# Kernel optimization log

Measured on AMD Instinct MI355X. Metric: run time of the kernel, lower is better.

## Reference

```python
import jax, jax.numpy as jnp
import numpy as np

DIM = 2048
N_HEADS = 32
N_KV_HEADS = 8
HEAD_DIM = 64
ROPE_BASE = 10000.0
BATCH = 2
SEQ = 2048


def apply_rope(x, cos, sin):
    # x: (B, S, H, hd); cos/sin: (1, S, 1, hd//2). Interleaved rotation.
    x1 = x[..., ::2]
    x2 = x[..., 1::2]
    r1 = x1 * cos - x2 * sin
    r2 = x1 * sin + x2 * cos
    return jnp.stack([r1, r2], axis=-1).reshape(x.shape)


def setup_inputs() -> dict:
    key = jax.random.key(0)
    ks = jax.random.split(key, 8)
    s = DIM ** -0.5
    x = jax.random.normal(ks[0], (BATCH, SEQ, DIM), dtype=jnp.float32)
    Wq = jax.random.normal(ks[1], (DIM, N_HEADS * HEAD_DIM), dtype=jnp.float32) * s
    Wk = jax.random.normal(ks[2], (DIM, N_KV_HEADS * HEAD_DIM), dtype=jnp.float32) * s
    Wv = jax.random.normal(ks[3], (DIM, N_KV_HEADS * HEAD_DIM), dtype=jnp.float32) * s
    bv = jax.random.normal(ks[4], (N_KV_HEADS * HEAD_DIM,), dtype=jnp.float32) * 0.01
    Wo = jax.random.normal(ks[5], (N_HEADS * HEAD_DIM, DIM), dtype=jnp.float32) * s
    bo = jax.random.normal(ks[6], (DIM,), dtype=jnp.float32) * 0.01
    # causal mask: 1 where attended, 0 where masked
    mask = jnp.tril(jnp.ones((SEQ, SEQ), dtype=jnp.int32))[None, None]
    return {"x": x, "Wq": Wq, "Wk": Wk, "Wv": Wv, "bv": bv, "Wo": Wo, "bo": bo, "mask": mask}


def reference(x, Wq, Wk, Wv, bv, Wo, bo, mask):
    B, S, _ = x.shape
    q = (x @ Wq).reshape(B, S, N_HEADS, HEAD_DIM)
    k = (x @ Wk).reshape(B, S, N_KV_HEADS, HEAD_DIM)
    v = (x @ Wv + bv).reshape(B, S, N_KV_HEADS, HEAD_DIM)

    # RoPE tables
    theta = 1.0 / ROPE_BASE ** (jnp.arange(0, HEAD_DIM, 2, dtype=jnp.float32) / HEAD_DIM)
    freqs = jnp.arange(S, dtype=jnp.float32)[:, None] * theta[None, :]  # (S, hd/2)
    cos = jnp.cos(freqs)[None, :, None, :]
    sin = jnp.sin(freqs)[None, :, None, :]

    q = apply_rope(q, cos, sin)
    k = apply_rope(k, cos, sin)

    rf = N_HEADS // N_KV_HEADS
    k = jnp.repeat(k, rf, axis=2)  # materialized GQA repeat, as in source
    v = jnp.repeat(v, rf, axis=2)

    scale = HEAD_DIM ** -0.5
    scores = jnp.einsum("bqhd,bkhd->bhqk", q, k) * scale  # (B, H, S, S)
    scores = jnp.where(mask == 0, -jnp.inf, scores)
    attn = jax.nn.softmax(scores, axis=-1)
    out = jnp.einsum("bhqk,bkhd->bqhd", attn, v).reshape(B, S, N_HEADS * HEAD_DIM)
    return out @ Wo + bo
```

## Files before the change

kernel.cpp:

```cpp
#include <hip/hip_runtime.h>
#include <hip/hip_bf16.h>

#define DIMX     2048
#define N_HEADS  32
#define N_KVH    8
#define HEAD_D   64
#define BATCH    2
#define SEQ      2048
#define M_ROWS   (BATCH * SEQ)
#define QKVN     3072
#define THETA_C  0.2878231366242557f
#define C1SCALE  0.1803368801111204f

typedef __attribute__((ext_vector_type(8))) short short8;
typedef __attribute__((ext_vector_type(4))) float f32x4;

#define DEV static __device__ __forceinline__

DEV float b2f(unsigned short u) { return __uint_as_float(((unsigned int)u) << 16); }
DEV unsigned short f2b(float f) {
  unsigned int x = __float_as_uint(f);
  return (unsigned short)((x + 0x7fffu + ((x >> 16) & 1u)) >> 16);
}
DEV unsigned int pk2(float lo, float hi) {
  __hip_bfloat162 h = __float22bfloat162_rn(make_float2(lo, hi));
  unsigned int u;
  __builtin_memcpy(&u, &h, 4);
  return u;
}
DEV void gld16(const void* g, void* lds) {
  __builtin_amdgcn_global_load_lds(
      (const __attribute__((address_space(1))) unsigned int*)g,
      (__attribute__((address_space(3))) unsigned int*)lds, 16, 0, 0);
}

__global__ void tab_k(float2* __restrict__ tab)
{
  int i = blockIdx.x * 256 + threadIdx.x;
  int s = i >> 5, j = i & 31;
  float th = __expf(-(float)j * THETA_C);
  float sn, cs;
  sincosf((float)s * th, &sn, &cs);
  tab[i] = make_float2(cs, sn);
}

__global__ void cast_k(const float* __restrict__ s, unsigned short* __restrict__ d, int n8)
{
  int i = blockIdx.x * 256 + threadIdx.x;
  if (i >= n8) return;
  float4 a = ((const float4*)s)[i * 2];
  float4 b = ((const float4*)s)[i * 2 + 1];
  uint4 o;
  o.x = pk2(a.x, a.y); o.y = pk2(a.z, a.w);
  o.z = pk2(b.x, b.y); o.w = pk2(b.z, b.w);
  ((uint4*)d)[i] = o;
}

__global__ __launch_bounds__(256) void transcast_k(
    const float* __restrict__ W, unsigned short* __restrict__ Wt, int Kd, int N)
{
  __shared__ float tile[64][65];
  const int t = threadIdx.x;
  const int k0 = blockIdx.y * 64, n0 = blockIdx.x * 64;
  const int r = t >> 4, c4 = (t & 15) << 2;
  #pragma unroll
  for (int pp = 0; pp < 4; ++pp) {
    float4 v = *(const float4*)(W + (size_t)(k0 + pp * 16 + r) * N + n0 + c4);
    *(float4*)&tile[pp * 16 + r][c4] = v;
  }
  __syncthreads();
  const int n = t >> 2, kc = (t & 3) << 4;
  uint4 u0, u1;
  u0.x = pk2(tile[kc + 0][n], tile[kc + 1][n]);
  u0.y = pk2(tile[kc + 2][n], tile[kc + 3][n]);
  u0.z = pk2(tile[kc + 4][n], tile[kc + 5][n]);
  u0.w = pk2(tile[kc + 6][n], tile[kc + 7][n]);
  u1.x = pk2(tile[kc + 8][n], tile[kc + 9][n]);
  u1.y = pk2(tile[kc + 10][n], tile[kc + 11][n]);
  u1.z = pk2(tile[kc + 12][n], tile[kc + 13][n]);
  u1.w = pk2(tile[kc + 14][n], tile[kc + 15][n]);
  unsigned short* dst = Wt + (size_t)(n0 + n) * Kd + k0 + kc;
  *(uint4*)dst = u0;
  *(uint4*)(dst + 8) = u1;
}

#define TM 128
#define TK 32

template<int OUTB>
__global__ __launch_bounds__(256) void gemm_bf16_k(
    const unsigned short* __restrict__ A,
    const unsigned short* __restrict__ Bt,
    const float* __restrict__ bias,
    void* __restrict__ Cp, int M, int N, int K)
{
  __shared__ unsigned short Al[TM * TK];
  __shared__ unsigned short Bl[TM * TK];
  const int t = threadIdx.x;
  const int l = t & 63, w = t >> 6;
  const int col = l & 15, grp = l >> 4;
  const int wr = (w >> 1) * 64, wc = (w & 1) * 64;

  const int gx = gridDim.x;
  const int lin = blockIdx.y * gx + blockIdx.x;
  const int wg = (lin & 7) * ((gx * gridDim.y) >> 3) + (lin >> 3);
  const int bm = (wg / gx) * 128, bn = (wg % gx) * 128;

  f32x4 acc[4][4];
  #pragma unroll
  for (int mi = 0; mi < 4; ++mi)
    #pragma unroll
    for (int ni = 0; ni < 4; ++ni) acc[mi][ni] = (f32x4){0.f, 0.f, 0.f, 0.f};

  const int lr = l >> 2;
  const int lc = (l & 3) * 8;
  const unsigned short* Aw = A + (size_t)(bm + w * 32 + lr) * K + lc;
  const unsigned short* Bw = Bt + (size_t)(bn + w * 32 + lr) * K + lc;
  unsigned short* Ald = &Al[(w * 32) * TK];
  unsigned short* Bld = &Bl[(w * 32) * TK];

  for (int k0 = 0; k0 < K; k0 += TK) {
    __syncthreads();
    gld16(Aw + k0, Ald);
    gld16(Aw + (size_t)16 * K + k0, Ald + 16 * TK);
    gld16(Bw + k0, Bld);
    gld16(Bw + (size_t)16 * K + k0, Bld + 16 * TK);
    __syncthreads();
    short8 af[4], bf[4];
    #pragma unroll
    for (int mi = 0; mi < 4; ++mi)
      af[mi] = *(const short8*)&Al[(wr + mi * 16 + col) * TK + grp * 8];
    #pragma unroll
    for (int ni = 0; ni < 4; ++ni)
      bf[ni] = *(const short8*)&Bl[(wc + ni * 16 + col) * TK + grp * 8];
    #pragma unroll
    for (int mi = 0; mi < 4; ++mi)
      #pragma unroll
      for (int ni = 0; ni < 4; ++ni)
        acc[mi][ni] = __builtin_amdgcn_mfma_f32_16x16x32_bf16(af[mi], bf[ni], acc[mi][ni], 0, 0, 0);
  }

  #pragma unroll
  for (int ni = 0; ni < 4; ++ni) {
    const int cn = bn + wc + ni * 16 + col;
    const float bvv = bias ? bias[cn] : 0.f;
    #pragma unroll
    for (int mi = 0; mi < 4; ++mi) {
      #pragma unroll
      for (int i = 0; i < 4; ++i) {
        const int cm = bm + wr + mi * 16 + grp * 4 + i;
        const float v = acc[mi][ni][i] + bvv;
        if (OUTB) ((unsigned short*)Cp)[(size_t)cm * N + cn] = f2b(v);
        else      ((float*)Cp)[(size_t)cm * N + cn] = v;
      }
    }
  }
}

__global__ void rope_b_k(unsigned short* __restrict__ qkv, const float2* __restrict__ tab)
{
  int i = blockIdx.x * 256 + threadIdx.x;
  unsigned short* p; int row, c8; float osc;
  if (i < M_ROWS * 256) {
    row = i >> 8; c8 = i & 255; osc = C1SCALE;
    p = qkv + (size_t)row * QKVN + c8 * 8;
  } else {
    i -= M_ROWS * 256;
    if (i >= M_ROWS * 64) return;
    row = i >> 6; c8 = i & 63; osc = 1.0f;
    p = qkv + (size_t)row * QKVN + 2048 + c8 * 8;
  }
  const int s = row & (SEQ - 1);
  const int j0 = (c8 & 7) * 4;
  short8 v = *(short8*)p;
  uint4 o;
  unsigned int ou[4];
  #pragma unroll
  for (int pp = 0; pp < 4; ++pp) {
    float2 cs = tab[(s << 5) + j0 + pp];
    float x1 = b2f((unsigned short)v[2 * pp]);
    float x2 = b2f((unsigned short)v[2 * pp + 1]);
    ou[pp] = pk2((x1 * cs.x - x2 * cs.y) * osc, (x1 * cs.y + x2 * cs.x) * osc);
  }
  o.x = ou[0]; o.y = ou[1]; o.z = ou[2]; o.w = ou[3];
  *(uint4*)p = o;
}

__global__ __launch_bounds__(256) void vt_cast_k(
    const unsigned short* __restrict__ qkv, const float* __restrict__ bv,
    unsigned short* __restrict__ vt)
{
  __shared__ unsigned short tile[64][72];
  const int t = threadIdx.x;
  const int s0 = blockIdx.x * 64, kvh = blockIdx.y, b = blockIdx.z;
  const int r = t >> 3, c = (t & 7) * 8;
  #pragma unroll
  for (int pp = 0; pp < 2; ++pp) {
    short8 vv = *(const short8*)(qkv + (size_t)(b * SEQ + s0 + r + pp * 32) * QKVN + 2560 + kvh * 64 + c);
    short8 ov;
    #pragma unroll
    for (int j = 0; j < 8; ++j)
      ov[j] = (short)f2b(b2f((unsigned short)vv[j]) + bv[kvh * 64 + c + j]);
    *(short8*)&tile[r + pp * 32][c] = ov;
  }
  __syncthreads();
  const int d = t >> 2, sc = (t & 3) * 16;
  short8 u0, u1;
  #pragma unroll
  for (int j = 0; j < 8; ++j) {
    const int p0 = sc + j, p1 = sc + 8 + j;
    u0[j] = (short)tile[(p0 & 3) * 16 + (p0 >> 2)][d];
    u1[j] = (short)tile[(p1 & 3) * 16 + (p1 >> 2)][d];
  }
  unsigned short* dst = vt + (size_t)((b * N_KVH + kvh) * 64 + d) * SEQ + s0 + sc;
  *(short8*)dst = u0;
  *(short8*)(dst + 8) = u1;
}

__global__ __launch_bounds__(256) void attn_mfma_k(
    const unsigned short* __restrict__ qkv,
    const unsigned short* __restrict__ vt,
    unsigned short* __restrict__ ob)
{
  __shared__ unsigned short P[4][32][72];
  const int t = threadIdx.x, l = t & 63, w = t >> 6;
  const int col = l & 15, grp = l >> 4;
  const int h = blockIdx.x, b = blockIdx.y;
  const int pairid = blockIdx.z * 4 + w;
  const int kvh = h >> 2;

  const unsigned short* kbase = qkv + (size_t)(b * SEQ) * QKVN + 2048 + kvh * 64;
  const unsigned short* vbase = vt + (size_t)((b * N_KVH + kvh) * 64) * SEQ;

  #pragma unroll
  for (int half = 0; half < 2; ++half) {
    const int strip = half ? (63 - pairid) : pairid;
    const int qr = strip * 32;

    short8 aq[2][2];
    #pragma unroll
    for (int j = 0; j < 2; ++j) {
      const unsigned short* qrow = qkv + (size_t)(b * SEQ + qr + j * 16 + col) * QKVN + h * 64;
      aq[j][0] = *(const short8*)(qrow + grp * 8);
      aq[j][1] = *(const short8*)(qrow + 32 + grp * 8);
    }

    f32x4 o[2][4];
    #pragma unroll
    for (int j = 0; j < 2; ++j)
      #pragma unroll
      for (int ti = 0; ti < 4; ++ti) o[j][ti] = (f32x4){0.f, 0.f, 0.f, 0.f};
    float ls[8];
    #pragma unroll
    for (int i = 0; i < 8; ++i) ls[i] = 0.f;

    const int wkend = qr + 32;

    for (int kt = 0; kt < wkend; kt += 64) {
      short8 kreg[8], vreg[8];
      #pragma unroll
      for (int ti = 0; ti < 4; ++ti) {
        const unsigned short* kr = kbase + (size_t)(kt + ti * 16 + col) * QKVN;
        kreg[ti * 2 + 0] = *(const short8*)(kr + grp * 8);
        kreg[ti * 2 + 1] = *(const short8*)(kr + 32 + grp * 8);
      }
      #pragma unroll
      for (int ti = 0; ti < 4; ++ti) {
        const unsigned short* vr = vbase + (size_t)(ti * 16 + col) * SEQ + kt + grp * 8;
        vreg[ti * 2 + 0] = *(const short8*)(vr);
        vreg[ti * 2 + 1] = *(const short8*)(vr + 32);
      }

      f32x4 sc[2][4];
      #pragma unroll
      for (int ti = 0; ti < 4; ++ti) {
        #pragma unroll
        for (int j = 0; j < 2; ++j) {
          f32x4 s = (f32x4){0.f, 0.f, 0.f, 0.f};
          s = __builtin_amdgcn_mfma_f32_16x16x32_bf16(aq[j][0], kreg[ti * 2 + 0], s, 0, 0, 0);
          s = __builtin_amdgcn_mfma_f32_16x16x32_bf16(aq[j][1], kreg[ti * 2 + 1], s, 0, 0, 0);
          sc[j][ti] = s;
        }
      }

      const bool diag = (kt + 32 >= qr);
      #pragma unroll
      for (int j = 0; j < 2; ++j) {
        #pragma unroll
        for (int i = 0; i < 4; ++i) {
          const int qg = qr + j * 16 + grp * 4 + i;
          float a0 = sc[j][0][i], a1 = sc[j][1][i], a2 = sc[j][2][i], a3 = sc[j][3][i];
          if (diag) {
            if (kt +  0 + col > qg) a0 = -1e30f;
            if (kt + 16 + col > qg) a1 = -1e30f;
            if (kt + 32 + col > qg) a2 = -1e30f;
            if (kt + 48 + col > qg) a3 = -1e30f;
          }
          float p0 = exp2f(a0), p1 = exp2f(a1);
          float p2 = exp2f(a2), p3 = exp2f(a3);
          ls[j * 4 + i] += (p0 + p1) + (p2 + p3);
          uint2 u;
          u.x = pk2(p0, p1);
          u.y = pk2(p2, p3);
          *(uint2*)&P[w][j * 16 + grp * 4 + i][col * 4] = u;
        }
      }

      #pragma unroll
      for (int kh = 0; kh < 2; ++kh) {
        short8 pa[2];
        #pragma unroll
        for (int j = 0; j < 2; ++j)
          pa[j] = *(const short8*)&P[w][j * 16 + col][kh * 32 + grp * 8];
        #pragma unroll
        for (int ti = 0; ti < 4; ++ti)
          #pragma unroll
          for (int j = 0; j < 2; ++j)
            o[j][ti] = __builtin_amdgcn_mfma_f32_16x16x32_bf16(pa[j], vreg[ti * 2 + kh], o[j][ti], 0, 0, 0);
      }
    }

    float inv[8];
    #pragma unroll
    for (int i = 0; i < 8; ++i) {
      float s = ls[i];
      #pragma unroll
      for (int off = 1; off < 16; off <<= 1) s += __shfl_xor(s, off);
      inv[i] = 1.0f / s;
    }

    #pragma unroll
    for (int j = 0; j < 2; ++j) {
      unsigned short* orow = ob + (size_t)(b * SEQ + qr + j * 16 + grp * 4) * 2048 + h * 64;
      #pragma unroll
      for (int ti = 0; ti < 4; ++ti)
        #pragma unroll
        for (int i = 0; i < 4; ++i)
          orow[(size_t)i * 2048 + ti * 16 + col] = f2b(o[j][ti][i] * inv[j * 4 + i]);
    }
  }
}

extern "C" void kernel_launch(void* const* d_in, const int* in_sizes, int n_in,
                              void* d_out, int out_size, void* d_ws, size_t ws_size,
                              hipStream_t stream)
{
  const float* x  = (const float*)d_in[0];
  const float* Wq = (const float*)d_in[1];
  const float* Wk = (const float*)d_in[2];
  const float* Wv = (const float*)d_in[3];
  const float* bv = (const float*)d_in[4];
  const float* Wo = (const float*)d_in[5];
  const float* bo = (const float*)d_in[6];
  float* out = (float*)d_out;

  unsigned short* p = (unsigned short*)d_ws;
  unsigned short* xb   = p; p += (size_t)M_ROWS * DIMX;
  unsigned short* Wqkt = p; p += (size_t)QKVN * DIMX;
  unsigned short* Wot  = p; p += (size_t)DIMX * DIMX;
  unsigned short* qkv  = p; p += (size_t)M_ROWS * QKVN;
  unsigned short* vtb  = p; p += (size_t)M_ROWS * 512;
  float2* tab = (float2*)p;  p += (size_t)SEQ * 32 * 4;
  unsigned short* ab = xb;

  tab_k<<<256, 256, 0, stream>>>(tab);
  cast_k<<<4096, 256, 0, stream>>>(x, xb, M_ROWS * DIMX / 8);
  transcast_k<<<dim3(32, 32), 256, 0, stream>>>(Wq, Wqkt,                       DIMX, 2048);
  transcast_k<<<dim3(8, 32),  256, 0, stream>>>(Wk, Wqkt + (size_t)2048 * DIMX, DIMX, 512);
  transcast_k<<<dim3(8, 32),  256, 0, stream>>>(Wv, Wqkt + (size_t)2560 * DIMX, DIMX, 512);
  transcast_k<<<dim3(32, 32), 256, 0, stream>>>(Wo, Wot,                        DIMX, 2048);

  gemm_bf16_k<1><<<dim3(QKVN / 128, M_ROWS / 128), 256, 0, stream>>>(
      xb, Wqkt, nullptr, qkv, M_ROWS, QKVN, DIMX);

  rope_b_k<<<5120, 256, 0, stream>>>(qkv, tab);
  vt_cast_k<<<dim3(32, 8, 2), 256, 0, stream>>>(qkv, bv, vtb);

  attn_mfma_k<<<dim3(N_HEADS, BATCH, 8), 256, 0, stream>>>(qkv, vtb, ab);

  gemm_bf16_k<0><<<dim3(DIMX / 128, M_ROWS / 128), 256, 0, stream>>>(
      ab, Wot, bo, out, M_ROWS, DIMX, DIMX);
}
```

Baseline: 398.5 us.

## Split attention key loop across two wave groups and combine partials in LDS

Doubles the attention block to 512 threads, with two waves per query strip each handling alternating 64-key tiles (split-K). The partial outputs and row sums from the first half are staged in shared memory and merged by the second half before normalization and store. The intent is more waves in flight and a shorter per-wave serial key loop. The cost is extra LDS for the combine buffers, two block-wide barriers per strip, and more register pressure at 512 threads. The kernel appears to use a fixed-max softmax (no running max), so adding the partial sums directly is valid.

```diff
diff --git a/kernel.cpp b/kernel.cpp
--- a/kernel.cpp
+++ b/kernel.cpp
@@ -217,16 +217,19 @@
   *(short8*)(dst + 8) = u1;
 }
 
-__global__ __launch_bounds__(256) void attn_mfma_k(
+__global__ __launch_bounds__(512) void attn_mfma_k(
     const unsigned short* __restrict__ qkv,
     const unsigned short* __restrict__ vt,
     unsigned short* __restrict__ ob)
 {
-  __shared__ unsigned short P[4][32][72];
+  __shared__ unsigned short P[8][32][72];
+  __shared__ float Ocomb[4][32][68];
+  __shared__ float Ls[4][32];
   const int t = threadIdx.x, l = t & 63, w = t >> 6;
   const int col = l & 15, grp = l >> 4;
+  const int pid = w & 3, hf = w >> 2;
   const int h = blockIdx.x, b = blockIdx.y;
-  const int pairid = blockIdx.z * 4 + w;
+  const int pairid = blockIdx.z * 4 + pid;
   const int kvh = h >> 2;
 
   const unsigned short* kbase = qkv + (size_t)(b * SEQ) * QKVN + 2048 + kvh * 64;
@@ -256,7 +259,7 @@
 
     const int wkend = qr + 32;
 
-    for (int kt = 0; kt < wkend; kt += 64) {
+    for (int kt = hf * 64; kt < wkend; kt += 128) {
       short8 kreg[8], vreg[8];
       #pragma unroll
       for (int ti = 0; ti < 4; ++ti) {
@@ -320,24 +323,51 @@
       }
     }
 
-    float inv[8];
+    float lsr[8];
     #pragma unroll
     for (int i = 0; i < 8; ++i) {
       float s = ls[i];
       #pragma unroll
       for (int off = 1; off < 16; off <<= 1) s += __shfl_xor(s, off);
-      inv[i] = 1.0f / s;
-    }
-
-    #pragma unroll
-    for (int j = 0; j < 2; ++j) {
-      unsigned short* orow = ob + (size_t)(b * SEQ + qr + j * 16 + grp * 4) * 2048 + h * 64;
-      #pragma unroll
-      for (int ti = 0; ti < 4; ++ti)
+      lsr[i] = s;
+    }
+
+    if (hf == 0) {
+      #pragma unroll
+      for (int j = 0; j < 2; ++j)
+        #pragma unroll
+        for (int ti = 0; ti < 4; ++ti)
+          #pragma unroll
+          for (int i = 0; i < 4; ++i)
+            Ocomb[pid][j * 16 + grp * 4 + i][ti * 16 + col] = o[j][ti][i];
+      if (col == 0) {
+        #pragma unroll
+        for (int j = 0; j < 2; ++j)
+          #pragma unroll
+          for (int i = 0; i < 4; ++i)
+            Ls[pid][j * 16 + grp * 4 + i] = lsr[j * 4 + i];
+      }
+    }
+    __syncthreads();
+    if (hf == 1) {
+      float inv[8];
+      #pragma unroll
+      for (int j = 0; j < 2; ++j)
         #pragma unroll
         for (int i = 0; i < 4; ++i)
-          orow[(size_t)i * 2048 + ti * 16 + col] = f2b(o[j][ti][i] * inv[j * 4 + i]);
-    }
+          inv[j * 4 + i] = 1.0f / (lsr[j * 4 + i] + Ls[pid][j * 16 + grp * 4 + i]);
+      #pragma unroll
+      for (int j = 0; j < 2; ++j) {
+        unsigned short* orow = ob + (size_t)(b * SEQ + qr + j * 16 + grp * 4) * 2048 + h * 64;
+        #pragma unroll
+        for (int ti = 0; ti < 4; ++ti)
+          #pragma unroll
+          for (int i = 0; i < 4; ++i)
+            orow[(size_t)i * 2048 + ti * 16 + col] =
+                f2b((o[j][ti][i] + Ocomb[pid][j * 16 + grp * 4 + i][ti * 16 + col]) * inv[j * 4 + i]);
+      }
+    }
+    __syncthreads();
   }
 }
 
@@ -376,7 +406,7 @@
   rope_b_k<<<5120, 256, 0, stream>>>(qkv, tab);
   vt_cast_k<<<dim3(32, 8, 2), 256, 0, stream>>>(qkv, bv, vtb);
 
-  attn_mfma_k<<<dim3(N_HEADS, BATCH, 8), 256, 0, stream>>>(qkv, vtb, ab);
+  attn_mfma_k<<<dim3(N_HEADS, BATCH, 8), 512, 0, stream>>>(qkv, vtb, ab);
 
   gemm_bf16_k<0><<<dim3(DIMX / 128, M_ROWS / 128), 256, 0, stream>>>(
       ab, Wot, bo, out, M_ROWS, DIMX, DIMX);
```

After: 400.5 us. Within noise of the previous version (+0.5%).
